# Performance work log

Hardware: AMD Instinct MI355X
Metric: run time of the kernel (lower is better)

The kernel has to match this reference:

```python
import jax, jax.numpy as jnp
import numpy as np

OUT, IN = 4096, 4096
B, S = 4, 2048


def setup_inputs() -> dict:
    key = jax.random.key(0)
    k_x, k_wh, k_wm, k_wl, k_r, k_s, k_b = jax.random.split(key, 7)
    x = jax.random.normal(k_x, (B, S, IN), dtype=jnp.float32)
    r = jax.random.uniform(k_r, (OUT, IN))
    high_mask = r < 0.2
    medium_mask = (r < 0.5) & ~high_mask
    weight_high = jax.random.normal(k_wh, (OUT, IN), dtype=jnp.float32) * 0.02 * high_mask
    weight_medium = (jax.random.normal(k_wm, (OUT, IN), dtype=jnp.float32) * 0.02 * medium_mask).astype(jnp.float16)
    weight_low = jax.random.randint(k_wl, (OUT, IN), -127, 128, dtype=jnp.int32)
    low_scale = jax.random.uniform(k_s, (1,), dtype=jnp.float32) * 0.001 + 1e-4
    bias = jax.random.normal(k_b, (OUT,), dtype=jnp.float32) * 0.02
    return {
        "x": x,
        "weight_high": weight_high,
        "weight_medium": weight_medium,
        "weight_low": weight_low,
        "high_precision_mask": high_mask,
        "medium_precision_mask": medium_mask,
        "low_scale": low_scale,
        "bias": bias,
    }


def reference(x, weight_high, weight_medium, weight_low,
              high_precision_mask, medium_precision_mask, low_scale, bias):
    # Reconstruct full fp32 weight from three precision tiers (as in forward).
    low_mask = ~high_precision_mask & ~medium_precision_mask
    w = (weight_high
         + medium_precision_mask * weight_medium.astype(jnp.float32)
         + low_mask * (weight_low.astype(jnp.float32) * low_scale[0]))
    # F.linear: x @ w.T + bias ; [B,S,IN] x [OUT,IN] -> [B,S,OUT]
    return jnp.einsum('bsi,oi->bso', x, w) + bias
```

## Files before the change

### kernel.cpp

```cpp
#include <hip/hip_runtime.h>
#include <hip/hip_bf16.h>
#include <hip/hip_fp16.h>


#define M_DIM 8192
#define N_DIM 4096
#define K_DIM 4096

typedef __attribute__((ext_vector_type(8))) short short8;
typedef __attribute__((ext_vector_type(4))) float floatx4;
typedef __attribute__((ext_vector_type(8))) _Float16 half8;
typedef __attribute__((ext_vector_type(8))) unsigned char uchar8;
typedef __attribute__((ext_vector_type(4))) int intx4;

__device__ inline unsigned short f2bf(float f) {
    union { float f; unsigned u; } v; v.f = f;
    return (unsigned short)((v.u + 0x7fffu + ((v.u >> 16) & 1u)) >> 16);
}

__device__ inline void async16(const void* g, const void* l) {
    __builtin_amdgcn_global_load_lds(
        (const __attribute__((address_space(1))) void*)g,
        (__attribute__((address_space(3))) void*)l,
        16, 0, 0);
}

__global__ __launch_bounds__(256) void prep_kernel(
        const float* __restrict__ x,
        const float* __restrict__ wh, const void* __restrict__ wm_raw,
        const int* __restrict__ wl, const void* __restrict__ hm_raw,
        const void* __restrict__ mm_raw, const float* __restrict__ scale_p,
        unsigned short* __restrict__ wbf, unsigned short* __restrict__ xbf) {
    const int bid = blockIdx.x;
    const int tid = threadIdx.x;

    if (bid >= 8192) {
        const size_t i = ((size_t)(bid - 8192) * 256 + tid) * 8;
        floatx4 f0 = *(const floatx4*)(x + i);
        floatx4 f1 = *(const floatx4*)(x + i + 4);
        short8 s;
        s[0] = (short)f2bf(f0[0]); s[1] = (short)f2bf(f0[1]);
        s[2] = (short)f2bf(f0[2]); s[3] = (short)f2bf(f0[3]);
        s[4] = (short)f2bf(f1[0]); s[5] = (short)f2bf(f1[1]);
        s[6] = (short)f2bf(f1[2]); s[7] = (short)f2bf(f1[3]);
        *(short8*)(xbf + i) = s;
        return;
    }

    const int lane = tid & 63;
    union { unsigned u; float f; } pw; pw.u = ((const unsigned*)wm_raw)[lane];
    const float pav = fabsf(pw.f);
    const bool wm_f32  = __popcll(__ballot(pav > 1e-4f && pav < 1.0f)) >= 4;
    const bool mask_u8 = __ballot(((const unsigned*)hm_raw)[lane] > 1u) != 0;

    const size_t i = ((size_t)bid * 256 + tid) * 8;
    const float scale = *scale_p;

    floatx4 h0 = *(const floatx4*)(wh + i);
    floatx4 h1 = *(const floatx4*)(wh + i + 4);
    intx4  l0 = *(const intx4*)(wl + i);
    intx4  l1 = *(const intx4*)(wl + i + 4);

    float mv[8];
    if (wm_f32) {
        floatx4 m0 = *(const floatx4*)((const float*)wm_raw + i);
        floatx4 m1 = *(const floatx4*)((const float*)wm_raw + i + 4);
#pragma unroll
        for (int e = 0; e < 4; ++e) { mv[e] = m0[e]; mv[e + 4] = m1[e]; }
    } else {
        half8 m = *(const half8*)((const _Float16*)wm_raw + i);
#pragma unroll
        for (int e = 0; e < 8; ++e) mv[e] = (float)m[e];
    }

    int lowmask[8];
    if (mask_u8) {
        uchar8 a = *(const uchar8*)((const unsigned char*)hm_raw + i);
        uchar8 b = *(const uchar8*)((const unsigned char*)mm_raw + i);
#pragma unroll
        for (int e = 0; e < 8; ++e) lowmask[e] = (a[e] | b[e]) == 0;
    } else {
        intx4 a0 = *(const intx4*)((const int*)hm_raw + i);
        intx4 a1 = *(const intx4*)((const int*)hm_raw + i + 4);
        intx4 b0 = *(const intx4*)((const int*)mm_raw + i);
        intx4 b1 = *(const intx4*)((const int*)mm_raw + i + 4);
#pragma unroll
        for (int e = 0; e < 4; ++e) {
            lowmask[e]     = (a0[e] | b0[e]) == 0;
            lowmask[e + 4] = (a1[e] | b1[e]) == 0;
        }
    }

    short8 s;
#pragma unroll
    for (int e = 0; e < 8; ++e) {
        float v = (e < 4 ? h0[e] : h1[e - 4]) + mv[e];
        int   lw = (e < 4 ? l0[e] : l1[e - 4]);
        if (lowmask[e]) v += (float)lw * scale;
        s[e] = (short)f2bf(v);
    }
    *(short8*)(wbf + i) = s;
}

__global__ __launch_bounds__(512, 2) void gemm256_kernel(
        const unsigned short* __restrict__ A,
        const unsigned short* __restrict__ Bw,
        const float* __restrict__ bias,
        float* __restrict__ out) {
    extern __shared__ char smem[];
    const int tid  = threadIdx.x;
    const int wave = tid >> 6, lane = tid & 63;
    const int lrow = lane & 15, lquad = lane >> 4;

    const int wg  = blockIdx.x;
    const int swz = (wg & 7) * 64 + (wg >> 3);
    const int bm0 = (swz >> 4) * 256;
    const int bn0 = (swz & 15) * 256;

    const int wr = wave >> 2, wc = wave & 3;
    const int wm = wr * 128, wn = wc * 64;

    const int lane2 = lane ^ ((lane & 32) ? 2 : 0);
    const int srow  = wave * 16 + (lane2 >> 2);
    const int scol  = (lane2 & 3) * 8;
    const unsigned short* gA0 = A  + (size_t)(bm0 + srow) * K_DIM + scol;
    const unsigned short* gA1 = gA0 + (size_t)128 * K_DIM;
    const unsigned short* gB0 = Bw + (size_t)(bn0 + srow) * K_DIM + scol;
    const unsigned short* gB1 = gB0 + (size_t)128 * K_DIM;
    const int dstS = wave * 1024;

    int offA[8], offB[4];
#pragma unroll
    for (int i = 0; i < 8; ++i) {
        int q = (wm + i * 16 + lrow) * 64 + lquad * 16;
        offA[i] = q ^ (((q >> 9) & 1) << 5);
    }
#pragma unroll
    for (int j = 0; j < 4; ++j) {
        int q = (wn + j * 16 + lrow) * 64 + lquad * 16;
        offB[j] = 16384 + (q ^ (((q >> 9) & 1) << 5));
    }

    floatx4 acc[8][4] = {};
    short8 afX[8], bqX[4], afY[8], bqY[4];

#define STAGE(T) do { \
        char* d_ = smem + ((T) & 3) * 32768 + dstS; \
        const unsigned ko_ = (unsigned)(T) * 32u; \
        async16(gA0 + ko_, d_); async16(gA1 + ko_, d_ + 8192); \
        async16(gB0 + ko_, d_ + 16384); async16(gB1 + ko_, d_ + 24576); } while (0)

#define RDS(AF, BQ, T) do { \
        const char* ab_ = smem + ((T) & 3) * 32768; \
        _Pragma("unroll") \
        for (int i_ = 0; i_ < 8; ++i_) AF[i_] = *(const short8*)(ab_ + offA[i_]); \
        _Pragma("unroll") \
        for (int j_ = 0; j_ < 4; ++j_) BQ[j_] = *(const short8*)(ab_ + offB[j_]); \
    } while (0)

#define MMA(AF, BQ) do { \
        __builtin_amdgcn_s_setprio(1); \
        _Pragma("unroll") \
        for (int i_ = 0; i_ < 8; ++i_) \
            _Pragma("unroll") \
            for (int j_ = 0; j_ < 4; ++j_) \
                acc[i_][j_] = __builtin_amdgcn_mfma_f32_16x16x32_bf16(AF[i_], BQ[j_], acc[i_][j_], 0, 0, 0); \
        __builtin_amdgcn_s_setprio(0); } while (0)

#define WAITV(n) asm volatile("s_waitcnt vmcnt(" #n ")" ::: "memory")
#define LGKM(n)  asm volatile("s_waitcnt lgkmcnt(" #n ")" ::: "memory")
#define BAR() do { __builtin_amdgcn_s_barrier(); asm volatile("" ::: "memory"); } while (0)
#define SCHED0() __builtin_amdgcn_sched_barrier(0)

#define ITER(T, AFC, BQC, AFN, BQN, DOB) do { \
        WAITV(4); \
        BAR(); \
        if (DOB) STAGE((T) + 3); \
        RDS(AFN, BQN, (T) + 1); \
        LGKM(12); \
        SCHED0(); \
        MMA(AFC, BQC); } while (0)

    STAGE(0); STAGE(1); STAGE(2);
    WAITV(8);
    BAR();
    RDS(afX, bqX, 0);

    const int NT = K_DIM / 32;
    for (int t = 0; t < NT - 4; t += 2) {
        ITER(t,     afX, bqX, afY, bqY, true);
        ITER(t + 1, afY, bqY, afX, bqX, true);
    }
    ITER(NT - 4, afX, bqX, afY, bqY, true);
    ITER(NT - 3, afY, bqY, afX, bqX, false);
    WAITV(0); BAR(); RDS(afY, bqY, NT - 1); LGKM(12); SCHED0(); MMA(afX, bqX);
    LGKM(0); SCHED0(); MMA(afY, bqY);

#undef STAGE
#undef RDS
#undef MMA
#undef WAITV
#undef LGKM
#undef BAR
#undef SCHED0
#undef ITER

#pragma unroll
    for (int j = 0; j < 4; ++j) {
        const int col = bn0 + wn + j * 16 + lrow;
        const float bv = bias[col];
#pragma unroll
        for (int i = 0; i < 8; ++i) {
            const int row = bm0 + wm + i * 16 + lquad * 4;
#pragma unroll
            for (int r = 0; r < 4; ++r)
                out[(size_t)(row + r) * N_DIM + col] = acc[i][j][r] + bv;
        }
    }
}

__global__ __launch_bounds__(256) void gemm_fused_kernel(
        const float* __restrict__ X,
        const unsigned short* __restrict__ Bw,
        const float* __restrict__ bias,
        float* __restrict__ out) {
    __shared__ unsigned short As[128 * 32];
    __shared__ unsigned short Bs[128 * 32];
    const int tid  = threadIdx.x;
    const int wave = tid >> 6, lane = tid & 63;
    const int bm0 = blockIdx.y * 128, bn0 = blockIdx.x * 128;
    const int wm = (wave >> 1) * 64, wn = (wave & 1) * 64;
    const int lrow = lane & 15, lquad = lane >> 4;
    const int arow = tid >> 1, acol = (tid & 1) * 16;

    floatx4 acc[4][4] = {};

    for (int k0 = 0; k0 < K_DIM; k0 += 32) {
        __syncthreads();
#pragma unroll
        for (int c = 0; c < 2; ++c) {
            const int lb  = wave * 2048 + c * 1024;
            const int e   = (lb >> 1) + lane * 8;
            const int row = e >> 5, col = e & 31;
            async16(Bw + (size_t)(bn0 + row) * K_DIM + k0 + col, (const char*)Bs + lb);
        }
        {
            const float* g = X + (size_t)(bm0 + arow) * K_DIM + k0 + acol;
            floatx4 f0 = *(const floatx4*)(g);
            floatx4 f1 = *(const floatx4*)(g + 4);
            floatx4 f2 = *(const floatx4*)(g + 8);
            floatx4 f3 = *(const floatx4*)(g + 12);
            short8 s0, s1;
            s0[0]=(short)f2bf(f0[0]); s0[1]=(short)f2bf(f0[1]); s0[2]=(short)f2bf(f0[2]); s0[3]=(short)f2bf(f0[3]);
            s0[4]=(short)f2bf(f1[0]); s0[5]=(short)f2bf(f1[1]); s0[6]=(short)f2bf(f1[2]); s0[7]=(short)f2bf(f1[3]);
            s1[0]=(short)f2bf(f2[0]); s1[1]=(short)f2bf(f2[1]); s1[2]=(short)f2bf(f2[2]); s1[3]=(short)f2bf(f2[3]);
            s1[4]=(short)f2bf(f3[0]); s1[5]=(short)f2bf(f3[1]); s1[6]=(short)f2bf(f3[2]); s1[7]=(short)f2bf(f3[3]);
            *(short8*)&As[arow * 32 + acol]     = s0;
            *(short8*)&As[arow * 32 + acol + 8] = s1;
        }
        __syncthreads();

        short8 af[4], bf[4];
#pragma unroll
        for (int i = 0; i < 4; ++i)
            af[i] = *(const short8*)&As[(wm + i * 16 + lrow) * 32 + lquad * 8];
#pragma unroll
        for (int j = 0; j < 4; ++j)
            bf[j] = *(const short8*)&Bs[(wn + j * 16 + lrow) * 32 + lquad * 8];
#pragma unroll
        for (int i = 0; i < 4; ++i)
#pragma unroll
            for (int j = 0; j < 4; ++j)
                acc[i][j] = __builtin_amdgcn_mfma_f32_16x16x32_bf16(af[i], bf[j], acc[i][j], 0, 0, 0);
    }

#pragma unroll
    for (int j = 0; j < 4; ++j) {
        const int col = bn0 + wn + j * 16 + lrow;
        const float bv = bias[col];
#pragma unroll
        for (int i = 0; i < 4; ++i) {
            const int row = bm0 + wm + i * 16 + lquad * 4;
#pragma unroll
            for (int r = 0; r < 4; ++r)
                out[(size_t)(row + r) * N_DIM + col] = acc[i][j][r] + bv;
        }
    }
}

extern "C" void kernel_launch(void* const* d_in, const int* in_sizes, int n_in,
                              void* d_out, int out_size, void* d_ws, size_t ws_size,
                              hipStream_t stream) {
    const float*    x     = (const float*)d_in[0];
    const float*    wh    = (const float*)d_in[1];
    const void*     wmed  = d_in[2];
    const int*      wl    = (const int*)d_in[3];
    const void*     hm    = d_in[4];
    const void*     mm    = d_in[5];
    const float*    scale = (const float*)d_in[6];
    const float*    bias  = (const float*)d_in[7];
    float*          out   = (float*)d_out;

    unsigned short* wbf   = (unsigned short*)((char*)d_ws + 256);
    unsigned short* xbf   = (unsigned short*)((char*)d_ws + 256 + (size_t)N_DIM * K_DIM * 2);
    const size_t need_full = 256 + (size_t)N_DIM * K_DIM * 2 + (size_t)M_DIM * K_DIM * 2;

    static bool attr_done = false;
    if (!attr_done) {
        (void)hipFuncSetAttribute(reinterpret_cast<const void*>(gemm256_kernel),
                                  hipFuncAttributeMaxDynamicSharedMemorySize, 131072);
        attr_done = true;
    }

    if (ws_size >= need_full) {
        prep_kernel<<<24576, 256, 0, stream>>>(x, wh, wmed, wl, hm, mm, scale, wbf, xbf);
        gemm256_kernel<<<dim3(512), dim3(512), 131072, stream>>>(xbf, wbf, bias, out);
    } else {
        prep_kernel<<<8192, 256, 0, stream>>>(x, wh, wmed, wl, hm, mm, scale, wbf, wbf);
        dim3 grid(N_DIM / 128, M_DIM / 128);
        gemm_fused_kernel<<<grid, 256, 0, stream>>>(x, wbf, bias, out);
    }
}
```

Measured before the change: 662.6 us.

## Replace 4-stage LDS pipeline with simple double-buffered K loop

Replaces the 4-deep LDS ring with register double-buffering of fragments with a plain 2-buffer scheme. Each iteration waits for all global loads, barriers, issues the next tile's load, then reads LDS and runs the MFMAs. LDS use drops from 128KB to 64KB, which could allow two blocks per CU. In exchange it loses overlap between LDS reads and MFMA and waits on vmcnt(0) every step, which exposes more load latency.

```diff
diff --git a/kernel.cpp b/kernel.cpp
--- a/kernel.cpp
+++ b/kernel.cpp
@@ -142,68 +142,51 @@
     }
 
     floatx4 acc[8][4] = {};
-    short8 afX[8], bqX[4], afY[8], bqY[4];
+    short8 af[8], bq[4];
 
 #define STAGE(T) do { \
-        char* d_ = smem + ((T) & 3) * 32768 + dstS; \
+        char* d_ = smem + ((T) & 1) * 32768 + dstS; \
         const unsigned ko_ = (unsigned)(T) * 32u; \
         async16(gA0 + ko_, d_); async16(gA1 + ko_, d_ + 8192); \
         async16(gB0 + ko_, d_ + 16384); async16(gB1 + ko_, d_ + 24576); } while (0)
 
-#define RDS(AF, BQ, T) do { \
-        const char* ab_ = smem + ((T) & 3) * 32768; \
+#define RDS(T) do { \
+        const char* ab_ = smem + ((T) & 1) * 32768; \
         _Pragma("unroll") \
-        for (int i_ = 0; i_ < 8; ++i_) AF[i_] = *(const short8*)(ab_ + offA[i_]); \
+        for (int i_ = 0; i_ < 8; ++i_) af[i_] = *(const short8*)(ab_ + offA[i_]); \
         _Pragma("unroll") \
-        for (int j_ = 0; j_ < 4; ++j_) BQ[j_] = *(const short8*)(ab_ + offB[j_]); \
+        for (int j_ = 0; j_ < 4; ++j_) bq[j_] = *(const short8*)(ab_ + offB[j_]); \
     } while (0)
 
-#define MMA(AF, BQ) do { \
+#define MMA() do { \
         __builtin_amdgcn_s_setprio(1); \
         _Pragma("unroll") \
         for (int i_ = 0; i_ < 8; ++i_) \
             _Pragma("unroll") \
             for (int j_ = 0; j_ < 4; ++j_) \
-                acc[i_][j_] = __builtin_amdgcn_mfma_f32_16x16x32_bf16(AF[i_], BQ[j_], acc[i_][j_], 0, 0, 0); \
+                acc[i_][j_] = __builtin_amdgcn_mfma_f32_16x16x32_bf16(af[i_], bq[j_], acc[i_][j_], 0, 0, 0); \
         __builtin_amdgcn_s_setprio(0); } while (0)
 
-#define WAITV(n) asm volatile("s_waitcnt vmcnt(" #n ")" ::: "memory")
-#define LGKM(n)  asm volatile("s_waitcnt lgkmcnt(" #n ")" ::: "memory")
+#define WAITV0() asm volatile("s_waitcnt vmcnt(0)" ::: "memory")
 #define BAR() do { __builtin_amdgcn_s_barrier(); asm volatile("" ::: "memory"); } while (0)
-#define SCHED0() __builtin_amdgcn_sched_barrier(0)
-
-#define ITER(T, AFC, BQC, AFN, BQN, DOB) do { \
-        WAITV(4); \
-        BAR(); \
-        if (DOB) STAGE((T) + 3); \
-        RDS(AFN, BQN, (T) + 1); \
-        LGKM(12); \
-        SCHED0(); \
-        MMA(AFC, BQC); } while (0)
-
-    STAGE(0); STAGE(1); STAGE(2);
-    WAITV(8);
-    BAR();
-    RDS(afX, bqX, 0);
+
+    STAGE(0);
 
     const int NT = K_DIM / 32;
-    for (int t = 0; t < NT - 4; t += 2) {
-        ITER(t,     afX, bqX, afY, bqY, true);
-        ITER(t + 1, afY, bqY, afX, bqX, true);
-    }
-    ITER(NT - 4, afX, bqX, afY, bqY, true);
-    ITER(NT - 3, afY, bqY, afX, bqX, false);
-    WAITV(0); BAR(); RDS(afY, bqY, NT - 1); LGKM(12); SCHED0(); MMA(afX, bqX);
-    LGKM(0); SCHED0(); MMA(afY, bqY);
+#pragma unroll 2
+    for (int t = 0; t < NT; ++t) {
+        WAITV0();
+        BAR();
+        if (t + 1 < NT) STAGE(t + 1);
+        RDS(t);
+        MMA();
+    }
 
 #undef STAGE
 #undef RDS
 #undef MMA
-#undef WAITV
-#undef LGKM
+#undef WAITV0
 #undef BAR
-#undef SCHED0
-#undef ITER
 
 #pragma unroll
     for (int j = 0; j < 4; ++j) {
@@ -308,13 +291,13 @@
     static bool attr_done = false;
     if (!attr_done) {
         (void)hipFuncSetAttribute(reinterpret_cast<const void*>(gemm256_kernel),
-                                  hipFuncAttributeMaxDynamicSharedMemorySize, 131072);
+                                  hipFuncAttributeMaxDynamicSharedMemorySize, 65536);
         attr_done = true;
     }
 
     if (ws_size >= need_full) {
         prep_kernel<<<24576, 256, 0, stream>>>(x, wh, wmed, wl, hm, mm, scale, wbf, xbf);
-        gemm256_kernel<<<dim3(512), dim3(512), 131072, stream>>>(xbf, wbf, bias, out);
+        gemm256_kernel<<<dim3(512), dim3(512), 65536, stream>>>(xbf, wbf, bias, out);
     } else {
         prep_kernel<<<8192, 256, 0, stream>>>(x, wh, wmed, wl, hm, mm, scale, wbf, wbf);
         dim3 grid(N_DIM / 128, M_DIM / 128);
```

Result: slower. 682.0 us (+2.9%).
